# Kernel optimization log

Hardware: AMD Instinct MI355X
Metric: run time of the kernel (lower is better)

The kernel has to match this reference:

```python
import jax, jax.numpy as jnp
import numpy as np

T, B, C = 2048, 8, 1024
H, K, PAD_L = 16, 31, 30
G = C // H


def setup_inputs() -> dict:
    key = jax.random.key(0)
    k1, k2 = jax.random.split(key)
    x = jax.random.normal(k1, (T, B, C), dtype=jnp.float32)
    # xavier_uniform for weight of shape (H, 1, K): fan_in=K, fan_out=H*... torch treats
    # dims as (out=H, in=1, receptive=K) -> fan_in=1*K, fan_out=H? Actually torch computes
    # fan_in = 1*K, fan_out = H*K for a (H,1,K) tensor is not right; torch: fan_in = in*rf = 1*K,
    # fan_out = out*rf = H*K? No: for (H,1,K), fan_in = 1*K, fan_out = H*K / H? Use standard formula:
    # fan_in = size(1)*K = K, fan_out = size(0)*K = H*K -> bound = sqrt(6/(K + H*K))
    bound = float(np.sqrt(6.0 / (K + H * K)))
    weight = jax.random.uniform(k2, (H, 1, K), dtype=jnp.float32, minval=-bound, maxval=bound)
    bias = jnp.zeros((C,), dtype=jnp.float32)
    return {"x": x, "weight": weight, "bias": bias}


def reference(x, weight, bias):
    # x: [T, B, C]; weight: [H, 1, K]; bias: [C]
    w = jax.nn.softmax(weight, axis=-1)  # per-head softmax over kernel taps
    # expand head weights to per-channel depthwise kernel: [C, 1, K]
    w_ch = jnp.repeat(w, G, axis=0)  # each of the G channels in head h shares w[h]
    xb = jnp.transpose(x, (1, 2, 0))  # [B, C, T]
    out = jax.lax.conv_general_dilated(
        xb, w_ch,
        window_strides=(1,),
        padding=[(PAD_L, 0)],  # left (causal) padding
        dimension_numbers=("NCH", "OIH", "NCH"),
        feature_group_count=C,
    )  # [B, C, T]
    out = jnp.transpose(out, (2, 0, 1))  # [T, B, C]
    return out + bias
```

## Files before the change

### kernel.cpp

```cpp
#include <hip/hip_runtime.h>
#include <stdint.h>

constexpr int T = 2048;
constexpr int B = 8;
constexpr int C = 1024;
constexpr int H = 16;
constexpr int K = 31;
constexpr int BC = B * C;

constexpr int TT = 64;
constexpr int NB = K - 1 + TT;
constexpr int BLOCK = 256;
constexpr int BLK_PER_CHUNK = BC / BLOCK;
constexpr int NCHUNK = T / TT;
constexpr int NBLK = BLK_PER_CHUNK * NCHUNK;

__global__ __launch_bounds__(BLOCK) void lconv_tbc_kernel(
        const float* __restrict__ x,
        const float* __restrict__ w,
        const float* __restrict__ bias,
        float* __restrict__ out) {
    const int tid = threadIdx.x;
    const int cb = blockIdx.x & (BLK_PER_CHUNK - 1);
    const int chunk = blockIdx.x / BLK_PER_CHUNK;
    const int bc = cb * BLOCK + tid;
    const int c = bc & (C - 1);
    const int h = __builtin_amdgcn_readfirstlane(c >> 6);

    const int t0 = chunk * TT;
    const float* col = x + bc;

    const float bi = bias[c];

    float buf[NB];
    if (chunk == 0) {
        #pragma unroll
        for (int j = 0; j < K - 1; ++j) buf[j] = 0.0f;
        #pragma unroll
        for (int j = K - 1; j < NB; ++j) {
            const float* a = col + (t0 + (j - (K - 1))) * BC;
            asm volatile("global_load_dword %0, %1, off"
                         : "=v"(buf[j]) : "v"(a));
        }
    } else {
        #pragma unroll
        for (int j = 0; j < NB; ++j) {
            const float* a = col + (t0 - (K - 1) + j) * BC;
            asm volatile("global_load_dword %0, %1, off"
                         : "=v"(buf[j]) : "v"(a));
        }
    }

    float tap[K];
    #pragma unroll
    for (int k = 0; k < K; ++k)
        tap[k] = __uint_as_float(__builtin_amdgcn_readfirstlane(
            __float_as_uint(w[h * K + k])));
    float m = tap[0];
    #pragma unroll
    for (int k = 1; k < K; ++k) m = fmaxf(m, tap[k]);
    float s = 0.0f;
    #pragma unroll
    for (int k = 0; k < K; ++k) s += __expf(tap[k] - m);
    const float inv = 1.0f / s;
    float wr[K];
    #pragma unroll
    for (int d = 0; d < K; ++d)
        wr[d] = __uint_as_float(__builtin_amdgcn_readfirstlane(
            __float_as_uint(__expf(tap[K - 1 - d] - m) * inv)));

    const int base = t0 * BC + bc;
    #pragma unroll
    for (int u = 0; u < TT; ++u) {
        float acc = bi;
        #pragma unroll
        for (int d = 0; d < K; ++d)
            acc = fmaf(wr[d], buf[K - 1 + u - d], acc);
        __builtin_nontemporal_store(acc, &out[base + u * BC]);
    }
}

extern "C" void kernel_launch(void* const* d_in, const int* in_sizes, int n_in,
                              void* d_out, int out_size, void* d_ws, size_t ws_size,
                              hipStream_t stream) {
    const float* x = (const float*)d_in[0];
    const float* w = (const float*)d_in[1];
    const float* bias = (const float*)d_in[2];
    float* out = (float*)d_out;

    lconv_tbc_kernel<<<dim3(NBLK), dim3(BLOCK), 0, stream>>>(x, w, bias, out);
}
```

Before: 31.19 us.

## Share causal halo between waves through LDS instead of reloading from global

Each block now covers 64 channels and 128 timesteps split across four waves of 32 timesteps. Only the first wave loads the 30-row halo from global memory. The other waves get their halo from the previous wave's loaded rows, passed through shared memory after a barrier. This removes most of the redundant halo reads, which were about 47% extra traffic with 64-step tiles. The cost is an LDS round trip, a block-wide sync, and a full vmcnt wait before any compute can start.

```diff
diff --git a/kernel.cpp b/kernel.cpp
--- a/kernel.cpp
+++ b/kernel.cpp
@@ -7,47 +7,56 @@
 constexpr int H = 16;
 constexpr int K = 31;
 constexpr int BC = B * C;
+constexpr int HALO = K - 1;
 
-constexpr int TT = 64;
-constexpr int NB = K - 1 + TT;
-constexpr int BLOCK = 256;
-constexpr int BLK_PER_CHUNK = BC / BLOCK;
-constexpr int NCHUNK = T / TT;
-constexpr int NBLK = BLK_PER_CHUNK * NCHUNK;
+constexpr int CPW = 64;
+constexpr int TW = 32;
+constexpr int WAVES = 4;
+constexpr int TBLK = TW * WAVES;
+constexpr int BLOCK = CPW * WAVES;
+constexpr int NCOL = BC / CPW;
+constexpr int NTCH = T / TBLK;
+constexpr int NBLK = NCOL * NTCH;
 
 __global__ __launch_bounds__(BLOCK) void lconv_tbc_kernel(
         const float* __restrict__ x,
         const float* __restrict__ w,
         const float* __restrict__ bias,
         float* __restrict__ out) {
+    __shared__ float hbuf[WAVES - 1][HALO][CPW];
+
     const int tid = threadIdx.x;
-    const int cb = blockIdx.x & (BLK_PER_CHUNK - 1);
-    const int chunk = blockIdx.x / BLK_PER_CHUNK;
-    const int bc = cb * BLOCK + tid;
+    const int wid = tid >> 6;
+    const int lane = tid & 63;
+    const int colslice = blockIdx.x & (NCOL - 1);
+    const int tch = blockIdx.x >> 7;
+    const int bc = colslice * CPW + lane;
     const int c = bc & (C - 1);
     const int h = __builtin_amdgcn_readfirstlane(c >> 6);
-
-    const int t0 = chunk * TT;
+    const int t0b = tch * TBLK;
+    const int tw = t0b + wid * TW;
     const float* col = x + bc;
 
     const float bi = bias[c];
 
-    float buf[NB];
-    if (chunk == 0) {
-        #pragma unroll
-        for (int j = 0; j < K - 1; ++j) buf[j] = 0.0f;
-        #pragma unroll
-        for (int j = K - 1; j < NB; ++j) {
-            const float* a = col + (t0 + (j - (K - 1))) * BC;
-            asm volatile("global_load_dword %0, %1, off"
-                         : "=v"(buf[j]) : "v"(a));
-        }
-    } else {
-        #pragma unroll
-        for (int j = 0; j < NB; ++j) {
-            const float* a = col + (t0 - (K - 1) + j) * BC;
-            asm volatile("global_load_dword %0, %1, off"
-                         : "=v"(buf[j]) : "v"(a));
+    float own[TW];
+    #pragma unroll
+    for (int j = 0; j < TW; ++j) {
+        const float* a = col + (tw + j) * BC;
+        asm volatile("global_load_dword %0, %1, off" : "=v"(own[j]) : "v"(a));
+    }
+    float hal[HALO];
+    if (wid == 0) {
+        if (tch == 0) {
+            #pragma unroll
+            for (int j = 0; j < HALO; ++j) hal[j] = 0.0f;
+        } else {
+            #pragma unroll
+            for (int j = 0; j < HALO; ++j) {
+                const float* a = col + (t0b - HALO + j) * BC;
+                asm volatile("global_load_dword %0, %1, off"
+                             : "=v"(hal[j]) : "v"(a));
+            }
         }
     }
 
@@ -69,13 +78,30 @@
         wr[d] = __uint_as_float(__builtin_amdgcn_readfirstlane(
             __float_as_uint(__expf(tap[K - 1 - d] - m) * inv)));
 
-    const int base = t0 * BC + bc;
+    asm volatile("s_waitcnt vmcnt(0)" ::: "memory");
+    __builtin_amdgcn_sched_barrier(0);
+    if (wid < WAVES - 1) {
+        #pragma unroll
+        for (int j = 0; j < HALO; ++j)
+            hbuf[wid][j][lane] = own[j + 2];
+    }
+    __syncthreads();
+    if (wid > 0) {
+        #pragma unroll
+        for (int j = 0; j < HALO; ++j)
+            hal[j] = hbuf[wid - 1][j][lane];
+    }
+
+    const int base = tw * BC + bc;
     #pragma unroll
-    for (int u = 0; u < TT; ++u) {
+    for (int u = 0; u < TW; ++u) {
         float acc = bi;
         #pragma unroll
-        for (int d = 0; d < K; ++d)
-            acc = fmaf(wr[d], buf[K - 1 + u - d], acc);
+        for (int d = 0; d < K; ++d) {
+            const int i = u - d;
+            const float v = (i >= 0) ? own[i] : hal[HALO + i];
+            acc = fmaf(wr[d], v, acc);
+        }
         __builtin_nontemporal_store(acc, &out[base + u * BC]);
     }
 }
```

Measured after the change: 29.45 us. 5.6% less time.
